# Optimization experiments

Hardware: AMD Instinct MI355X
Metric: run time of the kernel (lower is better)

Reference implementation:

```python
import jax, jax.numpy as jnp
import numpy as np

B, L, D = 16384, 32, 128
DIAG_LEN, PROC_LEN, MED_LEN = 100000, 50000, 1000


def setup_inputs() -> dict:
    key = jax.random.key(0)
    ks = jax.random.split(key, 12)
    inp = {
        "diag_codes": jax.random.randint(ks[0], (B, L), 0, DIAG_LEN),
        "proc_codes": jax.random.randint(ks[1], (B, L), 0, PROC_LEN),
        "prev_diag_codes": jax.random.randint(ks[2], (B, L), 0, DIAG_LEN),
        "prev_proc_codes": jax.random.randint(ks[3], (B, L), 0, PROC_LEN),
        # learned parameters (torch Linear convention: W[out,in], y = x @ W.T + b)
        "diag_emb": jax.random.normal(ks[4], (DIAG_LEN, D), jnp.float32) * 0.02,
        "proc_emb": jax.random.normal(ks[5], (PROC_LEN, D), jnp.float32) * 0.02,
        "W1": jax.random.normal(ks[6], (D, 2 * D), jnp.float32) * 0.02,
        "b1": jnp.zeros((D,), jnp.float32),
        "W2": jax.random.normal(ks[7], (256, 2 * D), jnp.float32) * 0.02,
        "b2": jnp.zeros((256,), jnp.float32),
        "W3": jax.random.normal(ks[8], (MED_LEN, 256), jnp.float32) * 0.02,
        "b3": jnp.zeros((MED_LEN,), jnp.float32),
    }
    return inp


def _bag_sum(table, idx):
    # EmbeddingBag('sum'): gather [B,L,D] then reduce over codes -> [B,D]
    return jnp.take(table, idx, axis=0).sum(axis=1)


def reference(diag_codes, proc_codes, prev_diag_codes, prev_proc_codes,
              diag_emb, proc_emb, W1, b1, W2, b2, W3, b3):
    emb_d = _bag_sum(diag_emb, diag_codes)            # [B,128]
    emb_p = _bag_sum(proc_emb, proc_codes)            # [B,128]
    prev_d = _bag_sum(diag_emb, prev_diag_codes)      # [B,128]
    prev_p = _bag_sum(proc_emb, prev_proc_codes)      # [B,128]

    # health_net = Linear(256->128) + Dropout (identity in eval mode)
    cur = jnp.concatenate([emb_d, emb_p], axis=1) @ W1.T + b1     # [B,128]
    prev = jnp.concatenate([prev_d, prev_p], axis=1) @ W1.T + b1  # [B,128]

    rep = jnp.concatenate([cur, prev], axis=1)        # [B,256]
    h = jax.nn.relu(rep @ W2.T + b2)                  # [B,256]
    return jax.nn.sigmoid(h @ W3.T + b3)              # [B,med_len]
```

## Files before the change

### kernel.cpp

```cpp
#include <hip/hip_runtime.h>
#include <hip/hip_bf16.h>
#include <math.h>

#define NB 16384
#define MED 1000
#define MD 100000
#define MP 50000
#define TDBLK 782
#define TPBLK 391
#define NTR (TDBLK + TPBLK)
#define NCV 1280
#define FP8_SCALE 4096.0f
#define FP8_INV   (1.0f / 4096.0f)

typedef __bf16 bf16x8 __attribute__((ext_vector_type(8)));
typedef float  f32x4  __attribute__((ext_vector_type(4)));
typedef float  f32x2  __attribute__((ext_vector_type(2)));
typedef unsigned short u16;
typedef unsigned int   u32;
typedef unsigned char  u8;

__device__ __forceinline__ u16 f2bf(float f) {
    union { float f; u32 u; } v; v.f = f;
    u32 r = v.u + 0x7fffu + ((v.u >> 16) & 1u);
    return (u16)(r >> 16);
}

__global__ __launch_bounds__(256) void prep_kernel(
    const float* __restrict__ Ed, const float* __restrict__ Ep,
    const float* __restrict__ W1,
    const float* __restrict__ W2, const float* __restrict__ W3,
    u8* __restrict__ Td, u8* __restrict__ Tp,
    u16* __restrict__ W2b, u16* __restrict__ W3b)
{
    __shared__ u16 w1s[128 * 132];
    const int bid = blockIdx.x, tid = threadIdx.x;

    if (bid >= NTR) {
        int i = (bid - NTR) * 256 + tid;
        if (i < 65536) { W2b[i] = f2bf(W2[i]); return; }
        i -= 65536;
        if (i < 262144) W3b[i] = (i < MED * 256) ? f2bf(W3[i]) : (u16)0;
        return;
    }

    int blk = bid;
    const float* E; u8* T; int M, koff;
    if (blk < TDBLK) { E = Ed; T = Td; M = MD; koff = 0; }
    else             { blk -= TDBLK; E = Ep; T = Tp; M = MP; koff = 128; }

    for (int idx = tid; idx < 4096; idx += 256) {
        const int row = idx >> 5, c4 = idx & 31;
        const float4 v = *(const float4*)(W1 + row * 256 + koff + c4 * 4);
        u16* d = &w1s[row * 132 + c4 * 4];
        d[0] = f2bf(v.x); d[1] = f2bf(v.y); d[2] = f2bf(v.z); d[3] = f2bf(v.w);
    }
    __syncthreads();

    const int wave = tid >> 6, lane = tid & 63;
    const int quad = lane >> 4, l16 = lane & 15;
    const int n0 = blk * 128 + wave * 32;
    const float* bP0 = E + (size_t)min(n0 + l16,      M - 1) * 128 + quad * 8;
    const float* bP1 = E + (size_t)min(n0 + 16 + l16, M - 1) * 128 + quad * 8;

    f32x4 acc[8][2];
    #pragma unroll
    for (int mt = 0; mt < 8; ++mt) {
        acc[mt][0] = (f32x4){0.f,0.f,0.f,0.f};
        acc[mt][1] = (f32x4){0.f,0.f,0.f,0.f};
    }

    #pragma unroll
    for (int ks = 0; ks < 4; ++ks) {
        union { bf16x8 v; u16 s[8]; } b0, b1;
        const float4 f0 = *(const float4*)(bP0 + ks * 32);
        const float4 f1 = *(const float4*)(bP0 + ks * 32 + 4);
        const float4 g0 = *(const float4*)(bP1 + ks * 32);
        const float4 g1 = *(const float4*)(bP1 + ks * 32 + 4);
        b0.s[0]=f2bf(f0.x); b0.s[1]=f2bf(f0.y); b0.s[2]=f2bf(f0.z); b0.s[3]=f2bf(f0.w);
        b0.s[4]=f2bf(f1.x); b0.s[5]=f2bf(f1.y); b0.s[6]=f2bf(f1.z); b0.s[7]=f2bf(f1.w);
        b1.s[0]=f2bf(g0.x); b1.s[1]=f2bf(g0.y); b1.s[2]=f2bf(g0.z); b1.s[3]=f2bf(g0.w);
        b1.s[4]=f2bf(g1.x); b1.s[5]=f2bf(g1.y); b1.s[6]=f2bf(g1.z); b1.s[7]=f2bf(g1.w);
        #pragma unroll
        for (int mt = 0; mt < 8; ++mt) {
            const bf16x8 a = *(const bf16x8*)&w1s[(mt * 16 + l16) * 132 + ks * 32 + quad * 8];
            acc[mt][0] = __builtin_amdgcn_mfma_f32_16x16x32_bf16(a, b0.v, acc[mt][0], 0, 0, 0);
            acc[mt][1] = __builtin_amdgcn_mfma_f32_16x16x32_bf16(a, b1.v, acc[mt][1], 0, 0, 0);
        }
    }

    #pragma unroll
    for (int nt = 0; nt < 2; ++nt) {
        const int rn = n0 + nt * 16 + l16;
        if (rn < M) {
            u8* rowp = T + (size_t)rn * 128 + quad * 4;
            #pragma unroll
            for (int mt = 0; mt < 8; ++mt) {
                const f32x4 a = acc[mt][nt];
                int p = __builtin_amdgcn_cvt_pk_fp8_f32(a[0] * FP8_SCALE, a[1] * FP8_SCALE, 0, 0);
                p = __builtin_amdgcn_cvt_pk_fp8_f32(a[2] * FP8_SCALE, a[3] * FP8_SCALE, p, 1);
                *(u32*)(rowp + mt * 16) = (u32)p;
            }
        }
    }
}

__global__ __launch_bounds__(256) void gather_rep(
    const int* __restrict__ diag, const int* __restrict__ proc,
    const int* __restrict__ pdiag, const int* __restrict__ pproc,
    const u8* __restrict__ Td, const u8* __restrict__ Tp,
    const float* __restrict__ b1, u16* __restrict__ rep)
{
    __shared__ int   sidx[528];
    __shared__ float sred[128][8];
    const int t = threadIdx.x;

    for (int i = t; i < 512; i += 256) {
        const int s = i >> 7, bg = (i >> 5) & 3, l = i & 31;
        const int* cp = (bg == 0) ? diag : (bg == 1) ? proc : (bg == 2) ? pdiag : pproc;
        sidx[s * 132 + bg * 33 + l] = cp[(blockIdx.x * 4 + s) * 32 + l];
    }
    __syncthreads();

    const int sub = t >> 6, bag = (t >> 4) & 3, lc = t & 15;
    const u8* tbl = (bag & 1) ? Tp : Td;
    const int* myidx = &sidx[sub * 132 + bag * 33];

    f32x2 s0 = {0.f,0.f}, s1 = {0.f,0.f}, s2 = {0.f,0.f}, s3 = {0.f,0.f};
    uint2 va[8], vb[8];
    #pragma unroll
    for (int j = 0; j < 8; ++j)
        va[j] = *(const uint2*)(tbl + (size_t)myidx[j] * 128 + lc * 8);
    #pragma unroll
    for (int j = 0; j < 8; ++j)
        vb[j] = *(const uint2*)(tbl + (size_t)myidx[8 + j] * 128 + lc * 8);

#define CONSUME(V) do { \
    _Pragma("unroll") \
    for (int j = 0; j < 8; ++j) { \
        s0 += __builtin_amdgcn_cvt_pk_f32_fp8((int)V[j].x, 0); \
        s1 += __builtin_amdgcn_cvt_pk_f32_fp8((int)V[j].x, 1); \
        s2 += __builtin_amdgcn_cvt_pk_f32_fp8((int)V[j].y, 0); \
        s3 += __builtin_amdgcn_cvt_pk_f32_fp8((int)V[j].y, 1); \
    } } while (0)

    {
        uint2 tmp[8];
        #pragma unroll
        for (int j = 0; j < 8; ++j)
            tmp[j] = *(const uint2*)(tbl + (size_t)myidx[16 + j] * 128 + lc * 8);
        CONSUME(va);
        #pragma unroll
        for (int j = 0; j < 8; ++j) va[j] = tmp[j];
    }
    {
        uint2 tmp[8];
        #pragma unroll
        for (int j = 0; j < 8; ++j)
            tmp[j] = *(const uint2*)(tbl + (size_t)myidx[24 + j] * 128 + lc * 8);
        CONSUME(vb);
        #pragma unroll
        for (int j = 0; j < 8; ++j) vb[j] = tmp[j];
    }
    CONSUME(va);
    CONSUME(vb);
#undef CONSUME

    const int oid = sub * 32 + (bag >> 1) * 16 + lc;
    if (bag & 1) {
        *(float4*)&sred[oid][0] = make_float4(s0.x, s0.y, s1.x, s1.y);
        *(float4*)&sred[oid][4] = make_float4(s2.x, s2.y, s3.x, s3.y);
    }
    __syncthreads();
    if (!(bag & 1)) {
        const float4 p0 = *(const float4*)&sred[oid][0];
        const float4 p1 = *(const float4*)&sred[oid][4];
        const float4 c0 = *(const float4*)(b1 + lc * 8);
        const float4 c1 = *(const float4*)(b1 + lc * 8 + 4);
        const float t0 = (s0.x + p0.x) * FP8_INV + c0.x;
        const float t1 = (s0.y + p0.y) * FP8_INV + c0.y;
        const float t2 = (s1.x + p0.z) * FP8_INV + c0.z;
        const float t3 = (s1.y + p0.w) * FP8_INV + c0.w;
        const float t4 = (s2.x + p1.x) * FP8_INV + c1.x;
        const float t5 = (s2.y + p1.y) * FP8_INV + c1.y;
        const float t6 = (s3.x + p1.z) * FP8_INV + c1.z;
        const float t7 = (s3.y + p1.w) * FP8_INV + c1.w;
        uint4 o;
        o.x = (u32)f2bf(t0) | ((u32)f2bf(t1) << 16);
        o.y = (u32)f2bf(t2) | ((u32)f2bf(t3) << 16);
        o.z = (u32)f2bf(t4) | ((u32)f2bf(t5) << 16);
        o.w = (u32)f2bf(t6) | ((u32)f2bf(t7) << 16);
        const int b = blockIdx.x * 4 + sub;
        *(uint4*)(rep + (size_t)b * 256 + (bag >> 1) * 128 + lc * 8) = o;
    }
}

__global__ __launch_bounds__(256) void gemm23(
    const u16* __restrict__ rep, const u16* __restrict__ W2b,
    const float* __restrict__ b2, const u16* __restrict__ W3b,
    const float* __restrict__ b3, float* __restrict__ out)
{
    __shared__ u16 hs[32][264];
    const int wave = threadIdx.x >> 6, lane = threadIdx.x & 63;
    const int quad = lane >> 4, l16 = lane & 15;
    const int mBase = blockIdx.x * 32;

    {
        const int mrow = mBase + (wave & 1) * 16 + l16;
        const int ncol0 = (wave >> 1) * 128;
        const u16* aP = rep + (size_t)mrow * 256 + quad * 8;
        bf16x8 a[8];
        #pragma unroll
        for (int ks = 0; ks < 8; ++ks) a[ks] = *(const bf16x8*)(aP + ks * 32);

        #pragma unroll
        for (int nt = 0; nt < 8; ++nt) {
            const int col = ncol0 + nt * 16 + l16;
            const u16* wP = W2b + (size_t)col * 256 + quad * 8;
            f32x4 acc = {0.f, 0.f, 0.f, 0.f};
            #pragma unroll
            for (int ks = 0; ks < 8; ++ks) {
                const bf16x8 b = *(const bf16x8*)(wP + ks * 32);
                acc = __builtin_amdgcn_mfma_f32_16x16x32_bf16(a[ks], b, acc, 0, 0, 0);
            }
            const float bv = b2[col];
            #pragma unroll
            for (int r = 0; r < 4; ++r) {
                float v = acc[r] + bv;
                v = v > 0.f ? v : 0.f;
                hs[(wave & 1) * 16 + quad * 4 + r][col] = f2bf(v);
            }
        }
    }
    __syncthreads();

    const int colW = wave * 256;
    #pragma unroll
    for (int nc = 0; nc < 4; ++nc) {
        f32x4 acc[2][4];
        #pragma unroll
        for (int mt = 0; mt < 2; ++mt)
            #pragma unroll
            for (int nti = 0; nti < 4; ++nti) acc[mt][nti] = (f32x4){0.f,0.f,0.f,0.f};

        #pragma unroll
        for (int ks = 0; ks < 8; ++ks) {
            bf16x8 af[2];
            #pragma unroll
            for (int mt = 0; mt < 2; ++mt)
                af[mt] = *(const bf16x8*)&hs[mt * 16 + l16][quad * 8 + ks * 32];
            #pragma unroll
            for (int nti = 0; nti < 4; ++nti) {
                const int wrow = colW + nc * 64 + nti * 16 + l16;
                const bf16x8 b = *(const bf16x8*)(W3b + (size_t)wrow * 256 + quad * 8 + ks * 32);
                acc[0][nti] = __builtin_amdgcn_mfma_f32_16x16x32_bf16(af[0], b, acc[0][nti], 0, 0, 0);
                acc[1][nti] = __builtin_amdgcn_mfma_f32_16x16x32_bf16(af[1], b, acc[1][nti], 0, 0, 0);
            }
        }
        #pragma unroll
        for (int nti = 0; nti < 4; ++nti) {
            const int col = colW + nc * 64 + nti * 16 + l16;
            if (col < MED) {
                const float bv = b3[col];
                #pragma unroll
                for (int mt = 0; mt < 2; ++mt) {
                    #pragma unroll
                    for (int r = 0; r < 4; ++r) {
                        const float v = acc[mt][nti][r] + bv;
                        out[(size_t)(mBase + mt * 16 + quad * 4 + r) * MED + col] =
                            1.0f / (1.0f + __expf(-v));
                    }
                }
            }
        }
    }
}

extern "C" void kernel_launch(void* const* d_in, const int* in_sizes, int n_in,
                              void* d_out, int out_size, void* d_ws, size_t ws_size,
                              hipStream_t stream)
{
    const int*   diag  = (const int*)d_in[0];
    const int*   proc  = (const int*)d_in[1];
    const int*   pdiag = (const int*)d_in[2];
    const int*   pproc = (const int*)d_in[3];
    const float* demb  = (const float*)d_in[4];
    const float* pemb  = (const float*)d_in[5];
    const float* W1    = (const float*)d_in[6];
    const float* b1    = (const float*)d_in[7];
    const float* W2    = (const float*)d_in[8];
    const float* b2    = (const float*)d_in[9];
    const float* W3    = (const float*)d_in[10];
    const float* b3    = (const float*)d_in[11];

    char* ws = (char*)d_ws;
    u8*  Td  = (u8*)ws;
    u8*  Tp  = (u8*)(ws + 12800000);
    u16* rep = (u16*)(ws + 19200000);
    u16* W2b = (u16*)(ws + 27588608);
    u16* W3b = (u16*)(ws + 27719680);

    prep_kernel<<<NTR + NCV, 256, 0, stream>>>(demb, pemb, W1, W2, W3, Td, Tp, W2b, W3b);
    gather_rep<<<NB / 4, 256, 0, stream>>>(diag, proc, pdiag, pproc, Td, Tp, b1, rep);
    gemm23<<<512, 256, 0, stream>>>(rep, W2b, b2, W3b, b3, (float*)d_out);
}
```

Before: 247.0 us.

## Split fused GEMM2/GEMM3 kernel into two kernels with 2D grid for GEMM3

Replaces the fused gemm23 kernel, which kept the ReLU hidden tile in shared memory, with two separate kernels. gemm2 writes the bf16 hidden activations to global workspace, reusing the region that held the fp8 tables. gemm3 then runs on a 256x8 grid of 64x128 output tiles. The aim is to raise parallelism in the dominant output GEMM beyond 512 blocks, at the cost of an extra global round trip for h and one more launch. It also relies on the Td region being dead once gather_rep has run.

```diff
diff --git a/kernel.cpp b/kernel.cpp
--- a/kernel.cpp
+++ b/kernel.cpp
@@ -195,81 +195,95 @@
     }
 }
 
-__global__ __launch_bounds__(256) void gemm23(
+__global__ __launch_bounds__(256) void gemm2(
     const u16* __restrict__ rep, const u16* __restrict__ W2b,
-    const float* __restrict__ b2, const u16* __restrict__ W3b,
-    const float* __restrict__ b3, float* __restrict__ out)
-{
-    __shared__ u16 hs[32][264];
+    const float* __restrict__ b2, u16* __restrict__ h)
+{
     const int wave = threadIdx.x >> 6, lane = threadIdx.x & 63;
     const int quad = lane >> 4, l16 = lane & 15;
     const int mBase = blockIdx.x * 32;
-
-    {
-        const int mrow = mBase + (wave & 1) * 16 + l16;
-        const int ncol0 = (wave >> 1) * 128;
-        const u16* aP = rep + (size_t)mrow * 256 + quad * 8;
-        bf16x8 a[8];
-        #pragma unroll
-        for (int ks = 0; ks < 8; ++ks) a[ks] = *(const bf16x8*)(aP + ks * 32);
-
-        #pragma unroll
-        for (int nt = 0; nt < 8; ++nt) {
-            const int col = ncol0 + nt * 16 + l16;
-            const u16* wP = W2b + (size_t)col * 256 + quad * 8;
-            f32x4 acc = {0.f, 0.f, 0.f, 0.f};
-            #pragma unroll
-            for (int ks = 0; ks < 8; ++ks) {
-                const bf16x8 b = *(const bf16x8*)(wP + ks * 32);
-                acc = __builtin_amdgcn_mfma_f32_16x16x32_bf16(a[ks], b, acc, 0, 0, 0);
-            }
+    const int nBase = wave * 64;
+    const u16* aP0 = rep + (size_t)(mBase + l16) * 256 + quad * 8;
+    const u16* aP1 = aP0 + 16 * 256;
+    const u16* wP  = W2b + (size_t)(nBase + l16) * 256 + quad * 8;
+
+    f32x4 acc[2][4];
+    #pragma unroll
+    for (int mt = 0; mt < 2; ++mt)
+        #pragma unroll
+        for (int nt = 0; nt < 4; ++nt) acc[mt][nt] = (f32x4){0.f,0.f,0.f,0.f};
+
+    #pragma unroll
+    for (int ks = 0; ks < 8; ++ks) {
+        const bf16x8 a0 = *(const bf16x8*)(aP0 + ks * 32);
+        const bf16x8 a1 = *(const bf16x8*)(aP1 + ks * 32);
+        #pragma unroll
+        for (int nt = 0; nt < 4; ++nt) {
+            const bf16x8 b = *(const bf16x8*)(wP + nt * 16 * 256 + ks * 32);
+            acc[0][nt] = __builtin_amdgcn_mfma_f32_16x16x32_bf16(a0, b, acc[0][nt], 0, 0, 0);
+            acc[1][nt] = __builtin_amdgcn_mfma_f32_16x16x32_bf16(a1, b, acc[1][nt], 0, 0, 0);
+        }
+    }
+
+    #pragma unroll
+    for (int mt = 0; mt < 2; ++mt) {
+        const int rowB = mBase + mt * 16 + quad * 4;
+        #pragma unroll
+        for (int nt = 0; nt < 4; ++nt) {
+            const int col = nBase + nt * 16 + l16;
             const float bv = b2[col];
             #pragma unroll
             for (int r = 0; r < 4; ++r) {
-                float v = acc[r] + bv;
+                float v = acc[mt][nt][r] + bv;
                 v = v > 0.f ? v : 0.f;
-                hs[(wave & 1) * 16 + quad * 4 + r][col] = f2bf(v);
+                h[(size_t)(rowB + r) * 256 + col] = f2bf(v);
             }
         }
     }
-    __syncthreads();
-
-    const int colW = wave * 256;
-    #pragma unroll
-    for (int nc = 0; nc < 4; ++nc) {
-        f32x4 acc[2][4];
-        #pragma unroll
-        for (int mt = 0; mt < 2; ++mt)
+}
+
+__global__ __launch_bounds__(256) void gemm3(
+    const u16* __restrict__ h, const u16* __restrict__ W3b,
+    const float* __restrict__ b3, float* __restrict__ out)
+{
+    const int wave = threadIdx.x >> 6, lane = threadIdx.x & 63;
+    const int quad = lane >> 4, l16 = lane & 15;
+    const int mBase = blockIdx.x * 64 + (wave & 1) * 32;
+    const int nBase = blockIdx.y * 128 + (wave >> 1) * 64;
+    const u16* aP0 = h + (size_t)(mBase + l16) * 256 + quad * 8;
+    const u16* aP1 = aP0 + 16 * 256;
+    const u16* wP  = W3b + (size_t)(nBase + l16) * 256 + quad * 8;
+
+    f32x4 acc[2][4];
+    #pragma unroll
+    for (int mt = 0; mt < 2; ++mt)
+        #pragma unroll
+        for (int nt = 0; nt < 4; ++nt) acc[mt][nt] = (f32x4){0.f,0.f,0.f,0.f};
+
+    #pragma unroll
+    for (int ks = 0; ks < 8; ++ks) {
+        const bf16x8 a0 = *(const bf16x8*)(aP0 + ks * 32);
+        const bf16x8 a1 = *(const bf16x8*)(aP1 + ks * 32);
+        #pragma unroll
+        for (int nt = 0; nt < 4; ++nt) {
+            const bf16x8 b = *(const bf16x8*)(wP + nt * 16 * 256 + ks * 32);
+            acc[0][nt] = __builtin_amdgcn_mfma_f32_16x16x32_bf16(a0, b, acc[0][nt], 0, 0, 0);
+            acc[1][nt] = __builtin_amdgcn_mfma_f32_16x16x32_bf16(a1, b, acc[1][nt], 0, 0, 0);
+        }
+    }
+
+    #pragma unroll
+    for (int nt = 0; nt < 4; ++nt) {
+        const int col = nBase + nt * 16 + l16;
+        if (col < MED) {
+            const float bv = b3[col];
             #pragma unroll
-            for (int nti = 0; nti < 4; ++nti) acc[mt][nti] = (f32x4){0.f,0.f,0.f,0.f};
-
-        #pragma unroll
-        for (int ks = 0; ks < 8; ++ks) {
-            bf16x8 af[2];
-            #pragma unroll
-            for (int mt = 0; mt < 2; ++mt)
-                af[mt] = *(const bf16x8*)&hs[mt * 16 + l16][quad * 8 + ks * 32];
-            #pragma unroll
-            for (int nti = 0; nti < 4; ++nti) {
-                const int wrow = colW + nc * 64 + nti * 16 + l16;
-                const bf16x8 b = *(const bf16x8*)(W3b + (size_t)wrow * 256 + quad * 8 + ks * 32);
-                acc[0][nti] = __builtin_amdgcn_mfma_f32_16x16x32_bf16(af[0], b, acc[0][nti], 0, 0, 0);
-                acc[1][nti] = __builtin_amdgcn_mfma_f32_16x16x32_bf16(af[1], b, acc[1][nti], 0, 0, 0);
-            }
-        }
-        #pragma unroll
-        for (int nti = 0; nti < 4; ++nti) {
-            const int col = colW + nc * 64 + nti * 16 + l16;
-            if (col < MED) {
-                const float bv = b3[col];
+            for (int mt = 0; mt < 2; ++mt) {
+                const int rowB = mBase + mt * 16 + quad * 4;
                 #pragma unroll
-                for (int mt = 0; mt < 2; ++mt) {
-                    #pragma unroll
-                    for (int r = 0; r < 4; ++r) {
-                        const float v = acc[mt][nti][r] + bv;
-                        out[(size_t)(mBase + mt * 16 + quad * 4 + r) * MED + col] =
-                            1.0f / (1.0f + __expf(-v));
-                    }
+                for (int r = 0; r < 4; ++r) {
+                    const float v = acc[mt][nt][r] + bv;
+                    out[(size_t)(rowB + r) * MED + col] = 1.0f / (1.0f + __expf(-v));
                 }
             }
         }
@@ -299,8 +313,10 @@
     u16* rep = (u16*)(ws + 19200000);
     u16* W2b = (u16*)(ws + 27588608);
     u16* W3b = (u16*)(ws + 27719680);
+    u16* h   = (u16*)ws;
 
     prep_kernel<<<NTR + NCV, 256, 0, stream>>>(demb, pemb, W1, W2, W3, Td, Tp, W2b, W3b);
     gather_rep<<<NB / 4, 256, 0, stream>>>(diag, proc, pdiag, pproc, Td, Tp, b1, rep);
-    gemm23<<<512, 256, 0, stream>>>(rep, W2b, b2, W3b, b3, (float*)d_out);
-}
+    gemm2<<<512, 256, 0, stream>>>(rep, W2b, b2, h);
+    gemm3<<<dim3(256, 8), 256, 0, stream>>>(h, W3b, b3, (float*)d_out);
+}
```

Result: slower. 255.3 us (+3.4%).
